# Optimization experiments

Hardware: AMD Instinct MI355X
Metric: run time of the kernel (lower is better)

The kernel has to match this reference:

```python
import jax, jax.numpy as jnp
import numpy as np

EMBED = 8   # forced: combine_heads Linear(embed_dim, embed_dim) applied to 8-wire measurement
FFN = 32
B, S = 128, 8192
EPS = 1e-5


def _layernorm(x, g, b):
    m = x.mean(-1, keepdims=True)
    v = ((x - m) ** 2).mean(-1, keepdims=True)
    return (x - m) * jax.lax.rsqrt(v + EPS) * g + b


def setup_inputs() -> dict:
    key = jax.random.key(0)
    ks = jax.random.split(key, 8)

    def lin(k, fi, fo):
        return jax.random.normal(k, (fi, fo), jnp.float32) / np.sqrt(fi).astype(np.float32)

    return dict(
        x=jax.random.normal(ks[0], (B, S, EMBED), jnp.float32),
        Wq=lin(ks[1], EMBED, EMBED), bq=jnp.zeros((EMBED,), jnp.float32),
        theta_attn=jax.random.uniform(ks[2], (EMBED,), jnp.float32, -np.pi, np.pi),
        Wc=lin(ks[3], EMBED, EMBED), bc=jnp.zeros((EMBED,), jnp.float32),
        g1=jnp.ones((EMBED,), jnp.float32), beta1=jnp.zeros((EMBED,), jnp.float32),
        theta_ffn=jax.random.uniform(ks[4], (EMBED,), jnp.float32, -np.pi, np.pi),
        W1=lin(ks[5], EMBED, FFN), b1=jnp.zeros((FFN,), jnp.float32),
        W2=lin(ks[6], FFN, EMBED), b2=jnp.zeros((EMBED,), jnp.float32),
        g2=jnp.ones((EMBED,), jnp.float32), beta2=jnp.zeros((EMBED,), jnp.float32),
    )


def reference(x, Wq, bq, theta_attn, Wc, bc, g1, beta1,
              theta_ffn, W1, b1, W2, b2, g2, beta2):
    # --- MultiHeadAttentionQuantum (eval mode, dropout = identity) ---
    # q_linear; the 8-wire encoder consumes all 8 features of q per token.
    q = x @ Wq + bq                           # [B, S, 8]
    # Circuit per token: RX(q_i) then trainable RX(theta_i) on wire i -> RX(q_i+theta_i),
    # then CNOT ring (0->1,...,6->7, 7->0), then <Z_i>.
    # All-RX product state => basis probs p_i(1)=sin^2(a_i/2); CNOTs permute basis
    # states (prefix-XOR of bits), so analytically:
    #   <Z_k> = prod_{j=0..k} cos(a_j)  for k>=1;   <Z_0> = prod_{j=1..7} cos(a_j)
    ca = jnp.cos(q + theta_attn)              # [B, S, 8]
    z_rest = jnp.cumprod(ca, axis=-1)[..., 1:]
    z0 = jnp.prod(ca[..., 1:], axis=-1, keepdims=True)
    z = jnp.concatenate([z0, z_rest], axis=-1)
    attn_out = z @ Wc + bc                    # combine_heads

    x1 = _layernorm(x + attn_out, g1, beta1)

    # --- FeedForwardQuantum: RX(x_i) then RY(theta_i), no entanglers ->
    #     <Z_i> = cos(theta_i) * cos(x_i)  (product state, per-wire closed form)
    zf = jnp.cos(theta_ffn) * jnp.cos(x1)     # [B, S, 8]
    h = jax.nn.relu(zf @ W1 + b1)             # linear1 -> relu
    ffn_out = h @ W2 + b2                     # linear2

    return _layernorm(x1 + ffn_out, g2, beta2)
```

## Files before the change

### kernel.cpp

```cpp
#include <hip/hip_runtime.h>


#define NTOK   (128 * 8192)
#define T      2
#define NTHREADS 256
#define NBLOCKS  (NTOK / (T * NTHREADS))
#define TSTRIDE  (NTOK / T)
#define LN_EPS 1e-5f
#define INV2PI 0.15915494309189535f

typedef __fp16 half2_t __attribute__((ext_vector_type(2)));

union PK { unsigned u; half2_t h; };

__device__ __forceinline__ float fast_cos_rev(float xrev) {
    return __builtin_amdgcn_cosf(xrev);
}
__device__ __forceinline__ float fast_cos(float x) {
    return __builtin_amdgcn_cosf(x * INV2PI);
}
__device__ __forceinline__ float fast_rsqrt(float x) {
    return __builtin_amdgcn_rsqf(x);
}
__device__ __forceinline__ unsigned packh2(float a, float b) {
    PK c; c.h = __builtin_amdgcn_cvt_pkrtz(a, b); return c.u;
}
__device__ __forceinline__ float dot2(half2_t a, unsigned bw, float c) {
    PK b; b.u = bw;
    return __builtin_amdgcn_fdot2(a, b.h, c, false);
}

__global__ void pack_weights(const float* __restrict__ Wq,
                             const float* __restrict__ W1,
                             const float* __restrict__ W2,
                             const float* __restrict__ Wc,
                             const float* __restrict__ bq,
                             const float* __restrict__ tha,
                             unsigned* __restrict__ ws)
{
    int idx = threadIdx.x;
    if (idx < 32) {
        int k = idx >> 2, p = idx & 3;
        ws[idx] = packh2(Wq[(2 * p) * 8 + k] * INV2PI, Wq[(2 * p + 1) * 8 + k] * INV2PI);
    } else if (idx < 160) {
        int i2 = idx - 32;
        int m = i2 >> 2, p = i2 & 3;
        ws[idx] = packh2(W1[(2 * p) * 32 + m], W1[(2 * p + 1) * 32 + m]);
    } else if (idx < 288) {
        int i2 = idx - 160;
        int mp = i2 >> 3, j = i2 & 7;
        ws[idx] = packh2(W2[(2 * mp) * 8 + j], W2[(2 * mp + 1) * 8 + j]);
    } else if (idx < 320) {
        int i2 = idx - 288;
        int kp = i2 >> 3, j = i2 & 7;
        ws[idx] = packh2(Wc[(2 * kp) * 8 + j], Wc[(2 * kp + 1) * 8 + j]);
    } else if (idx < 328) {
        int k = idx - 320;
        ws[idx] = __float_as_uint((bq[k] + tha[k]) * INV2PI);
    }
}

__global__ __launch_bounds__(NTHREADS, 8)
void qtb_kernel(const float* __restrict__ x,
                const float* __restrict__ bc,
                const float* __restrict__ g1,  const float* __restrict__ be1,
                const float* __restrict__ thf,
                const float* __restrict__ b1,
                const float* __restrict__ b2,
                const float* __restrict__ g2,  const float* __restrict__ be2,
                const unsigned* __restrict__ wp,
                float* __restrict__ out)
{
    const int g = blockIdx.x * NTHREADS + threadIdx.x;
    const float* qb = reinterpret_cast<const float*>(wp + 320);

    float xv[T][8];
    half2_t xp[T][4];
#pragma unroll
    for (int t = 0; t < T; ++t) {
        const float4* p = reinterpret_cast<const float4*>(x) + (size_t)(t * TSTRIDE + g) * 2;
        float4 a = p[0];
        float4 b = p[1];
        xv[t][0] = a.x; xv[t][1] = a.y; xv[t][2] = a.z; xv[t][3] = a.w;
        xv[t][4] = b.x; xv[t][5] = b.y; xv[t][6] = b.z; xv[t][7] = b.w;
        xp[t][0] = __builtin_amdgcn_cvt_pkrtz(a.x, a.y);
        xp[t][1] = __builtin_amdgcn_cvt_pkrtz(a.z, a.w);
        xp[t][2] = __builtin_amdgcn_cvt_pkrtz(b.x, b.y);
        xp[t][3] = __builtin_amdgcn_cvt_pkrtz(b.z, b.w);
    }

    float ca[T][8];
#pragma unroll
    for (int k = 0; k < 8; ++k) {
        const float bqk = qb[k];
#pragma unroll
        for (int t = 0; t < T; ++t) {
            float q = bqk;
#pragma unroll
            for (int p = 0; p < 4; ++p) q = dot2(xp[t][p], wp[k * 4 + p], q);
            ca[t][k] = fast_cos_rev(q);
        }
    }

    float attn[T][8];
#pragma unroll
    for (int t = 0; t < T; ++t)
#pragma unroll
        for (int j = 0; j < 8; ++j) attn[t][j] = bc[j];
#pragma unroll
    for (int t = 0; t < T; ++t) {
        float z[8];
        float cp  = ca[t][0];
        float cp1 = 1.0f;
#pragma unroll
        for (int k = 1; k < 8; ++k) {
            cp  *= ca[t][k];
            cp1 *= ca[t][k];
            z[k] = cp;
        }
        z[0] = cp1;
        half2_t zp[4];
#pragma unroll
        for (int p = 0; p < 4; ++p)
            zp[p] = __builtin_amdgcn_cvt_pkrtz(z[2 * p], z[2 * p + 1]);
#pragma unroll
        for (int p = 0; p < 4; ++p)
#pragma unroll
            for (int j = 0; j < 8; ++j)
                attn[t][j] = dot2(zp[p], wp[288 + p * 8 + j], attn[t][j]);
    }

    float cf[8];
#pragma unroll
    for (int j = 0; j < 8; ++j) cf[j] = fast_cos(thf[j]);
    float sg1[8], sb1[8];
#pragma unroll
    for (int j = 0; j < 8; ++j) { sg1[j] = g1[j]; sb1[j] = be1[j]; }

    half2_t zfp[T][4];
#pragma unroll
    for (int t = 0; t < T; ++t) {
        float y[8];
        float s = 0.f;
#pragma unroll
        for (int j = 0; j < 8; ++j) { y[j] = xv[t][j] + attn[t][j]; s += y[j]; }
        float m = s * 0.125f;
        float v = 0.f;
#pragma unroll
        for (int j = 0; j < 8; ++j) { float d = y[j] - m; v += d * d; }
        float r = fast_rsqrt(v * 0.125f + LN_EPS);
        float zf[8];
#pragma unroll
        for (int j = 0; j < 8; ++j) {
            float x1 = (y[j] - m) * r * sg1[j] + sb1[j];
            xv[t][j] = x1;
            zf[j] = cf[j] * fast_cos(x1);
        }
#pragma unroll
        for (int p = 0; p < 4; ++p)
            zfp[t][p] = __builtin_amdgcn_cvt_pkrtz(zf[2 * p], zf[2 * p + 1]);
    }

    float ffn[T][8];
    {
        float sb2[8];
#pragma unroll
        for (int j = 0; j < 8; ++j) sb2[j] = b2[j];
#pragma unroll
        for (int t = 0; t < T; ++t)
#pragma unroll
            for (int j = 0; j < 8; ++j) ffn[t][j] = sb2[j];
    }
#pragma unroll
    for (int mp = 0; mp < 16; ++mp) {
        const int m0 = 2 * mp, m1 = 2 * mp + 1;
        const float b1a = b1[m0];
        const float b1b = b1[m1];
        unsigned w2p[8];
#pragma unroll
        for (int j = 0; j < 8; ++j) w2p[j] = wp[160 + mp * 8 + j];
#pragma unroll
        for (int t = 0; t < T; ++t) {
            float h0 = b1a, h1 = b1b;
#pragma unroll
            for (int p = 0; p < 4; ++p) {
                h0 = dot2(zfp[t][p], wp[32 + m0 * 4 + p], h0);
                h1 = dot2(zfp[t][p], wp[32 + m1 * 4 + p], h1);
            }
            h0 = fmaxf(h0, 0.f);
            h1 = fmaxf(h1, 0.f);
            half2_t hp = __builtin_amdgcn_cvt_pkrtz(h0, h1);
#pragma unroll
            for (int j = 0; j < 8; ++j) ffn[t][j] = dot2(hp, w2p[j], ffn[t][j]);
        }
    }

    float sg2[8], sbb2[8];
#pragma unroll
    for (int j = 0; j < 8; ++j) { sg2[j] = g2[j]; sbb2[j] = be2[j]; }
#pragma unroll
    for (int t = 0; t < T; ++t) {
        float y[8];
        float s = 0.f;
#pragma unroll
        for (int j = 0; j < 8; ++j) { y[j] = xv[t][j] + ffn[t][j]; s += y[j]; }
        float m = s * 0.125f;
        float v = 0.f;
#pragma unroll
        for (int j = 0; j < 8; ++j) { float d = y[j] - m; v += d * d; }
        float r = fast_rsqrt(v * 0.125f + LN_EPS);
        float o[8];
#pragma unroll
        for (int j = 0; j < 8; ++j) o[j] = (y[j] - m) * r * sg2[j] + sbb2[j];
        float4* q = reinterpret_cast<float4*>(out) + (size_t)(t * TSTRIDE + g) * 2;
        q[0] = make_float4(o[0], o[1], o[2], o[3]);
        q[1] = make_float4(o[4], o[5], o[6], o[7]);
    }
}

extern "C" void kernel_launch(void* const* d_in, const int* in_sizes, int n_in,
                              void* d_out, int out_size, void* d_ws, size_t ws_size,
                              hipStream_t stream) {
    (void)in_sizes; (void)n_in; (void)ws_size; (void)out_size;
    unsigned* wp = (unsigned*)d_ws;
    pack_weights<<<1, 384, 0, stream>>>(
        (const float*)d_in[1],
        (const float*)d_in[9],
        (const float*)d_in[11],
        (const float*)d_in[4],
        (const float*)d_in[2],
        (const float*)d_in[3],
        wp);
    qtb_kernel<<<NBLOCKS, NTHREADS, 0, stream>>>(
        (const float*)d_in[0],
        (const float*)d_in[5],
        (const float*)d_in[6],
        (const float*)d_in[7],
        (const float*)d_in[8],
        (const float*)d_in[10],
        (const float*)d_in[12],
        (const float*)d_in[13],
        (const float*)d_in[14],
        wp,
        (float*)d_out);
}
```

Measured before the change: 123.8 us.

## Move FFN matmuls to MFMA 16x16x32 f16 with LDS staging per wave

The FFN's two small matmuls (8->32 and 32->8) now run on MFMA 16x16x32 f16 instructions instead of per-thread fdot2 chains. Each wave stages its packed activations, hidden ReLU outputs and FFN outputs through shared memory to move data between the per-token thread layout and the MFMA fragment layouts. The weights are repacked into fragment-shaped uint4 tiles, and each thread now handles one token instead of two, with the launch-bounds occupancy hint lowered. This is meant to cut the VALU cost of the FFN but adds LDS round trips and zero-padded MFMA work.

Result: faster. 114.9 us (-7.2%).

```diff
diff --git a/kernel.cpp b/kernel.cpp
--- a/kernel.cpp
+++ b/kernel.cpp
@@ -2,16 +2,17 @@
 
 
 #define NTOK   (128 * 8192)
-#define T      2
 #define NTHREADS 256
-#define NBLOCKS  (NTOK / (T * NTHREADS))
-#define TSTRIDE  (NTOK / T)
+#define NBLOCKS  (NTOK / NTHREADS)
 #define LN_EPS 1e-5f
 #define INV2PI 0.15915494309189535f
 
 typedef __fp16 half2_t __attribute__((ext_vector_type(2)));
-
-union PK { unsigned u; half2_t h; };
+typedef __fp16 half8_t __attribute__((ext_vector_type(8)));
+typedef float  float4_t __attribute__((ext_vector_type(4)));
+
+union PK  { unsigned u; half2_t h; };
+union U4H { uint4 u; half8_t h; half2_t h2[4]; };
 
 __device__ __forceinline__ float fast_cos_rev(float xrev) {
     return __builtin_amdgcn_cosf(xrev);
@@ -42,25 +43,38 @@
     if (idx < 32) {
         int k = idx >> 2, p = idx & 3;
         ws[idx] = packh2(Wq[(2 * p) * 8 + k] * INV2PI, Wq[(2 * p + 1) * 8 + k] * INV2PI);
-    } else if (idx < 160) {
+    } else if (idx < 64) {
         int i2 = idx - 32;
-        int m = i2 >> 2, p = i2 & 3;
-        ws[idx] = packh2(W1[(2 * p) * 32 + m], W1[(2 * p + 1) * 32 + m]);
-    } else if (idx < 288) {
-        int i2 = idx - 160;
-        int mp = i2 >> 3, j = i2 & 7;
-        ws[idx] = packh2(W2[(2 * mp) * 8 + j], W2[(2 * mp + 1) * 8 + j]);
-    } else if (idx < 320) {
-        int i2 = idx - 288;
         int kp = i2 >> 3, j = i2 & 7;
         ws[idx] = packh2(Wc[(2 * kp) * 8 + j], Wc[(2 * kp + 1) * 8 + j]);
-    } else if (idx < 328) {
-        int k = idx - 320;
+    } else if (idx < 72) {
+        int k = idx - 64;
         ws[idx] = __float_as_uint((bq[k] + tha[k]) * INV2PI);
-    }
-}
-
-__global__ __launch_bounds__(NTHREADS, 8)
+    } else if (idx >= 128 && idx < 320) {
+        int t  = (idx - 128) & 63;
+        int tb = (idx - 128) >> 6;
+        int n0 = t & 15, q = t >> 4;
+        uint4 w = make_uint4(0u, 0u, 0u, 0u);
+        unsigned r[4] = {0u, 0u, 0u, 0u};
+        if (tb == 0) {
+            if (q == 0)
+                for (int p = 0; p < 4; ++p)
+                    r[p] = packh2(W1[(2 * p) * 32 + n0], W1[(2 * p + 1) * 32 + n0]);
+        } else if (tb == 1) {
+            if (q == 0)
+                for (int p = 0; p < 4; ++p)
+                    r[p] = packh2(W1[(2 * p) * 32 + n0 + 16], W1[(2 * p + 1) * 32 + n0 + 16]);
+        } else {
+            if (n0 < 8)
+                for (int p = 0; p < 4; ++p)
+                    r[p] = packh2(W2[(8 * q + 2 * p) * 8 + n0], W2[(8 * q + 2 * p + 1) * 8 + n0]);
+        }
+        w.x = r[0]; w.y = r[1]; w.z = r[2]; w.w = r[3];
+        reinterpret_cast<uint4*>(ws)[32 + tb * 64 + t] = w;
+    }
+}
+
+__global__ __launch_bounds__(NTHREADS, 4)
 void qtb_kernel(const float* __restrict__ x,
                 const float* __restrict__ bc,
                 const float* __restrict__ g1,  const float* __restrict__ be1,
@@ -71,51 +85,60 @@
                 const unsigned* __restrict__ wp,
                 float* __restrict__ out)
 {
-    const int g = blockIdx.x * NTHREADS + threadIdx.x;
-    const float* qb = reinterpret_cast<const float*>(wp + 320);
-
-    float xv[T][8];
-    half2_t xp[T][4];
-#pragma unroll
-    for (int t = 0; t < T; ++t) {
-        const float4* p = reinterpret_cast<const float4*>(x) + (size_t)(t * TSTRIDE + g) * 2;
+    const int tid  = threadIdx.x;
+    const int wave = tid >> 6;
+    const int lane = tid & 63;
+    const int col  = lane & 15;
+    const int quad = lane >> 4;
+    const int g    = blockIdx.x * NTHREADS + tid;
+    const float* qb = reinterpret_cast<const float*>(wp + 64);
+
+    __shared__ uint4 zbuf[4][64];
+    __shared__ float hbuf[4][16 * 34];
+    __shared__ float fbuf[4][64 * 9];
+
+    const uint4* fr = reinterpret_cast<const uint4*>(wp);
+    U4H B1a, B1b, B2;
+    B1a.u = fr[32 + lane];
+    B1b.u = fr[96 + lane];
+    B2.u  = fr[160 + lane];
+    const float b1a_s = b1[col];
+    const float b1b_s = b1[col + 16];
+    const float b2_s  = (col < 8) ? b2[col & 7] : 0.f;
+
+    float xv[8];
+    half2_t xp[4];
+    {
+        const float4* p = reinterpret_cast<const float4*>(x) + (size_t)g * 2;
         float4 a = p[0];
         float4 b = p[1];
-        xv[t][0] = a.x; xv[t][1] = a.y; xv[t][2] = a.z; xv[t][3] = a.w;
-        xv[t][4] = b.x; xv[t][5] = b.y; xv[t][6] = b.z; xv[t][7] = b.w;
-        xp[t][0] = __builtin_amdgcn_cvt_pkrtz(a.x, a.y);
-        xp[t][1] = __builtin_amdgcn_cvt_pkrtz(a.z, a.w);
-        xp[t][2] = __builtin_amdgcn_cvt_pkrtz(b.x, b.y);
-        xp[t][3] = __builtin_amdgcn_cvt_pkrtz(b.z, b.w);
-    }
-
-    float ca[T][8];
+        xv[0] = a.x; xv[1] = a.y; xv[2] = a.z; xv[3] = a.w;
+        xv[4] = b.x; xv[5] = b.y; xv[6] = b.z; xv[7] = b.w;
+        xp[0] = __builtin_amdgcn_cvt_pkrtz(a.x, a.y);
+        xp[1] = __builtin_amdgcn_cvt_pkrtz(a.z, a.w);
+        xp[2] = __builtin_amdgcn_cvt_pkrtz(b.x, b.y);
+        xp[3] = __builtin_amdgcn_cvt_pkrtz(b.z, b.w);
+    }
+
+    float ca[8];
 #pragma unroll
     for (int k = 0; k < 8; ++k) {
-        const float bqk = qb[k];
-#pragma unroll
-        for (int t = 0; t < T; ++t) {
-            float q = bqk;
-#pragma unroll
-            for (int p = 0; p < 4; ++p) q = dot2(xp[t][p], wp[k * 4 + p], q);
-            ca[t][k] = fast_cos_rev(q);
-        }
-    }
-
-    float attn[T][8];
-#pragma unroll
-    for (int t = 0; t < T; ++t)
-#pragma unroll
-        for (int j = 0; j < 8; ++j) attn[t][j] = bc[j];
-#pragma unroll
-    for (int t = 0; t < T; ++t) {
+        float q = qb[k];
+#pragma unroll
+        for (int p = 0; p < 4; ++p) q = dot2(xp[p], wp[k * 4 + p], q);
+        ca[k] = fast_cos_rev(q);
+    }
+    float attn[8];
+#pragma unroll
+    for (int j = 0; j < 8; ++j) attn[j] = bc[j];
+    {
         float z[8];
-        float cp  = ca[t][0];
+        float cp  = ca[0];
         float cp1 = 1.0f;
 #pragma unroll
         for (int k = 1; k < 8; ++k) {
-            cp  *= ca[t][k];
-            cp1 *= ca[t][k];
+            cp  *= ca[k];
+            cp1 *= ca[k];
             z[k] = cp;
         }
         z[0] = cp1;
@@ -127,23 +150,14 @@
         for (int p = 0; p < 4; ++p)
 #pragma unroll
             for (int j = 0; j < 8; ++j)
-                attn[t][j] = dot2(zp[p], wp[288 + p * 8 + j], attn[t][j]);
-    }
-
-    float cf[8];
-#pragma unroll
-    for (int j = 0; j < 8; ++j) cf[j] = fast_cos(thf[j]);
-    float sg1[8], sb1[8];
-#pragma unroll
-    for (int j = 0; j < 8; ++j) { sg1[j] = g1[j]; sb1[j] = be1[j]; }
-
-    half2_t zfp[T][4];
-#pragma unroll
-    for (int t = 0; t < T; ++t) {
+                attn[j] = dot2(zp[p], wp[32 + p * 8 + j], attn[j]);
+    }
+
+    {
         float y[8];
         float s = 0.f;
 #pragma unroll
-        for (int j = 0; j < 8; ++j) { y[j] = xv[t][j] + attn[t][j]; s += y[j]; }
+        for (int j = 0; j < 8; ++j) { y[j] = xv[j] + attn[j]; s += y[j]; }
         float m = s * 0.125f;
         float v = 0.f;
 #pragma unroll
@@ -152,58 +166,53 @@
         float zf[8];
 #pragma unroll
         for (int j = 0; j < 8; ++j) {
-            float x1 = (y[j] - m) * r * sg1[j] + sb1[j];
-            xv[t][j] = x1;
-            zf[j] = cf[j] * fast_cos(x1);
-        }
+            float x1 = (y[j] - m) * r * g1[j] + be1[j];
+            xv[j] = x1;
+            zf[j] = fast_cos(thf[j]) * fast_cos(x1);
+        }
+        U4H zpk;
 #pragma unroll
         for (int p = 0; p < 4; ++p)
-            zfp[t][p] = __builtin_amdgcn_cvt_pkrtz(zf[2 * p], zf[2 * p + 1]);
-    }
-
-    float ffn[T][8];
-    {
-        float sb2[8];
-#pragma unroll
-        for (int j = 0; j < 8; ++j) sb2[j] = b2[j];
-#pragma unroll
-        for (int t = 0; t < T; ++t)
-#pragma unroll
-            for (int j = 0; j < 8; ++j) ffn[t][j] = sb2[j];
-    }
-#pragma unroll
-    for (int mp = 0; mp < 16; ++mp) {
-        const int m0 = 2 * mp, m1 = 2 * mp + 1;
-        const float b1a = b1[m0];
-        const float b1b = b1[m1];
-        unsigned w2p[8];
-#pragma unroll
-        for (int j = 0; j < 8; ++j) w2p[j] = wp[160 + mp * 8 + j];
-#pragma unroll
-        for (int t = 0; t < T; ++t) {
-            float h0 = b1a, h1 = b1b;
-#pragma unroll
-            for (int p = 0; p < 4; ++p) {
-                h0 = dot2(zfp[t][p], wp[32 + m0 * 4 + p], h0);
-                h1 = dot2(zfp[t][p], wp[32 + m1 * 4 + p], h1);
-            }
-            h0 = fmaxf(h0, 0.f);
-            h1 = fmaxf(h1, 0.f);
-            half2_t hp = __builtin_amdgcn_cvt_pkrtz(h0, h1);
-#pragma unroll
-            for (int j = 0; j < 8; ++j) ffn[t][j] = dot2(hp, w2p[j], ffn[t][j]);
-        }
-    }
-
-    float sg2[8], sbb2[8];
-#pragma unroll
-    for (int j = 0; j < 8; ++j) { sg2[j] = g2[j]; sbb2[j] = be2[j]; }
-#pragma unroll
-    for (int t = 0; t < T; ++t) {
+            zpk.h2[p] = __builtin_amdgcn_cvt_pkrtz(zf[2 * p], zf[2 * p + 1]);
+        zbuf[wave][lane] = zpk.u;
+    }
+
+#pragma unroll
+    for (int grp = 0; grp < 4; ++grp) {
+        U4H A1; A1.u = zbuf[wave][grp * 16 + col];
+        float4_t c1a = {b1a_s, b1a_s, b1a_s, b1a_s};
+        float4_t c1b = {b1b_s, b1b_s, b1b_s, b1b_s};
+        float4_t h0 = __builtin_amdgcn_mfma_f32_16x16x32_f16(A1.h, B1a.h, c1a, 0, 0, 0);
+        float4_t h1 = __builtin_amdgcn_mfma_f32_16x16x32_f16(A1.h, B1b.h, c1b, 0, 0, 0);
+#pragma unroll
+        for (int r = 0; r < 4; ++r) {
+            hbuf[wave][(4 * quad + r) * 34 + col]      = fmaxf(h0[r], 0.f);
+            hbuf[wave][(4 * quad + r) * 34 + col + 16] = fmaxf(h1[r], 0.f);
+        }
+        U4H A2;
+#pragma unroll
+        for (int p = 0; p < 4; ++p) {
+            float ha = hbuf[wave][col * 34 + 8 * quad + 2 * p];
+            float hb = hbuf[wave][col * 34 + 8 * quad + 2 * p + 1];
+            A2.h2[p] = __builtin_amdgcn_cvt_pkrtz(ha, hb);
+        }
+        float4_t c2 = {b2_s, b2_s, b2_s, b2_s};
+        float4_t f = __builtin_amdgcn_mfma_f32_16x16x32_f16(A2.h, B2.h, c2, 0, 0, 0);
+        if (col < 8) {
+#pragma unroll
+            for (int r = 0; r < 4; ++r)
+                fbuf[wave][(grp * 16 + 4 * quad + r) * 9 + col] = f[r];
+        }
+    }
+
+    {
         float y[8];
         float s = 0.f;
 #pragma unroll
-        for (int j = 0; j < 8; ++j) { y[j] = xv[t][j] + ffn[t][j]; s += y[j]; }
+        for (int j = 0; j < 8; ++j) {
+            y[j] = xv[j] + fbuf[wave][lane * 9 + j];
+            s += y[j];
+        }
         float m = s * 0.125f;
         float v = 0.f;
 #pragma unroll
@@ -211,8 +220,8 @@
         float r = fast_rsqrt(v * 0.125f + LN_EPS);
         float o[8];
 #pragma unroll
-        for (int j = 0; j < 8; ++j) o[j] = (y[j] - m) * r * sg2[j] + sbb2[j];
-        float4* q = reinterpret_cast<float4*>(out) + (size_t)(t * TSTRIDE + g) * 2;
+        for (int j = 0; j < 8; ++j) o[j] = (y[j] - m) * r * g2[j] + be2[j];
+        float4* q = reinterpret_cast<float4*>(out) + (size_t)g * 2;
         q[0] = make_float4(o[0], o[1], o[2], o[3]);
         q[1] = make_float4(o[4], o[5], o[6], o[7]);
     }
@@ -223,7 +232,7 @@
                               hipStream_t stream) {
     (void)in_sizes; (void)n_in; (void)ws_size; (void)out_size;
     unsigned* wp = (unsigned*)d_ws;
-    pack_weights<<<1, 384, 0, stream>>>(
+    pack_weights<<<1, 320, 0, stream>>>(
         (const float*)d_in[1],
         (const float*)d_in[9],
         (const float*)d_in[11],
```
